# Optimization experiments

Measured on AMD Instinct MI355X. Metric: run time of the kernel, lower is better.

The kernel has to match this reference:

```python
import jax, jax.numpy as jnp
import numpy as np

B, N, F_IN, C_OUT = 128, 512, 2, 64
C_IN = F_IN + C_OUT           # 66, concat(input, state) feature dim
MLP_IN = (2 * 3 + 1) * C_IN   # order=2, support_len=3 -> 462


def _gcn(x, supports, W, b):
    """Diffusion conv: x [B,N,F]; for each support a, 2 diffusion orders."""
    outs = [x]
    for a in supports:
        x1 = jnp.einsum('bnf,nm->bmf', x, a)
        x2 = jnp.einsum('bnf,nm->bmf', x1, a)
        outs += [x1, x2]
    h = jnp.concatenate(outs, axis=2)  # [B, N, 7*F]
    return h @ W + b                   # Linear (dropout is eval-mode identity)


def setup_inputs() -> dict:
    key = jax.random.key(0)
    ks = jax.random.split(key, 12)
    return {
        'input': jax.random.normal(ks[0], (B, N, F_IN), dtype=jnp.float32),
        'state': jax.random.normal(ks[1], (B, N, C_OUT), dtype=jnp.float32),
        'A0':    jax.random.uniform(ks[2], (N, N), dtype=jnp.float32),
        'A1':    jax.random.uniform(ks[3], (N, N), dtype=jnp.float32),
        'nv1_1': jax.random.normal(ks[4], (N, 10), dtype=jnp.float32),
        'nv2_1': jax.random.normal(ks[5], (10, N), dtype=jnp.float32),
        'W1':    jax.random.normal(ks[6], (MLP_IN, 2 * C_OUT), dtype=jnp.float32) * 0.02,
        'b1':    jnp.zeros((2 * C_OUT,), dtype=jnp.float32),
        'nv1_2': jax.random.normal(ks[7], (N, 10), dtype=jnp.float32),
        'nv2_2': jax.random.normal(ks[8], (10, N), dtype=jnp.float32),
        'W2':    jax.random.normal(ks[9], (MLP_IN, C_OUT), dtype=jnp.float32) * 0.02,
        'b2':    jnp.zeros((C_OUT,), dtype=jnp.float32),
    }


def reference(input, state, A0, A1, nv1_1, nv2_1, W1, b1, nv1_2, nv2_2, W2, b2):
    c_out = state.shape[-1]
    # gcn_1: adaptive adjacency + diffusion conv, then sigmoid gating split into r,u
    adp1 = jax.nn.softmax(jax.nn.relu(nv1_1 @ nv2_1), axis=1)
    x = jnp.concatenate([input, state], axis=2)
    value = jax.nn.sigmoid(_gcn(x, [A0, A1, adp1], W1, b1))
    r, u = value[..., :c_out], value[..., c_out:]
    # gcn_2: candidate state
    adp2 = jax.nn.softmax(jax.nn.relu(nv1_2 @ nv2_2), axis=1)
    x2 = jnp.concatenate([input, r * state], axis=2)
    c = jnp.tanh(_gcn(x2, [A0, A1, adp2], W2, b2))
    return u * state + (1.0 - u) * c
```

## Files before the change

kernel.cpp:

```cpp
#include <hip/hip_runtime.h>
#include <math.h>

#define NN 512
#define BB 128
#define CIN 66
#define QQ (BB*CIN)
#define AN ((size_t)NN*NN)
#define HB 480
#define KTOT 480

typedef unsigned short ushort_t;
typedef __attribute__((ext_vector_type(8))) short short8;
typedef __attribute__((ext_vector_type(8))) unsigned short us8;
typedef __attribute__((ext_vector_type(4))) float f32x4;
typedef __attribute__((ext_vector_type(4))) unsigned short us4;

__device__ __forceinline__ size_t pidx(int b, int frow, int n) {
    return ((size_t)(b * 30 + (frow >> 4)) << 13) + ((size_t)(n >> 3) << 7)
         + ((frow & 15) << 3) + (n & 7);
}

__device__ __forceinline__ ushort_t f2bf(float f) {
    unsigned u = __float_as_uint(f);
    u += 0x7FFF + ((u >> 16) & 1);
    return (ushort_t)(u >> 16);
}
__device__ __forceinline__ float bf2f(ushort_t h) {
    return __uint_as_float(((unsigned)h) << 16);
}
__device__ __forceinline__ void split_bf(float f, ushort_t& hi, ushort_t& lo) {
    hi = f2bf(f);
    lo = f2bf(f - bf2f(hi));
}
__device__ __forceinline__ void gload_lds16(const void* g, void* l) {
    __builtin_amdgcn_global_load_lds(
        (const __attribute__((address_space(1))) unsigned*)g,
        (__attribute__((address_space(3))) unsigned*)l, 16, 0, 0);
}

__global__ __launch_bounds__(512) void adp_kernel(const float* __restrict__ nv1,
                                                  const float* __restrict__ nv2,
                                                  float* __restrict__ adp) {
    int n = blockIdx.x;
    int m = threadIdx.x;
    float z = 0.f;
#pragma unroll
    for (int k = 0; k < 10; k++) z = fmaf(nv1[n * 10 + k], nv2[k * NN + m], z);
    z = fmaxf(z, 0.f);

    __shared__ float sred[8];
    int wid  = threadIdx.x >> 6;
    int lane = threadIdx.x & 63;

    float v = z;
#pragma unroll
    for (int off = 32; off; off >>= 1) v = fmaxf(v, __shfl_down(v, off, 64));
    if (lane == 0) sred[wid] = v;
    __syncthreads();
    float zmax = sred[0];
#pragma unroll
    for (int i = 1; i < 8; i++) zmax = fmaxf(zmax, sred[i]);

    float e = __expf(z - zmax);
    __syncthreads();
    v = e;
#pragma unroll
    for (int off = 32; off; off >>= 1) v += __shfl_down(v, off, 64);
    if (lane == 0) sred[wid] = v;
    __syncthreads();
    float tot = 0.f;
#pragma unroll
    for (int i = 0; i < 8; i++) tot += sred[i];

    adp[n * NN + m] = e / tot;
}

__global__ __launch_bounds__(256) void asplit_kernel(const float* __restrict__ A0,
                                                     const float* __restrict__ A1,
                                                     const float* __restrict__ P1,
                                                     const float* __restrict__ P2,
                                                     ushort_t* __restrict__ Ahi,
                                                     ushort_t* __restrict__ Alo) {
    __shared__ float t[32][33];
    int s = blockIdx.z;
    const float* src = (s == 0) ? A0 : (s == 1) ? A1 : (s == 2) ? P1 : P2;
    int m0 = blockIdx.x * 32, k0 = blockIdx.y * 32;
    int tx = threadIdx.x & 31, ty = threadIdx.x >> 5;
#pragma unroll
    for (int r = 0; r < 32; r += 8)
        t[ty + r][tx] = src[(size_t)(k0 + ty + r) * NN + m0 + tx];
    __syncthreads();
#pragma unroll
    for (int r = 0; r < 32; r += 8) {
        int m = m0 + ty + r, k = k0 + tx;
        float v = t[tx][ty + r];
        ushort_t h, l; split_bf(v, h, l);
        int mt = m >> 4, l15 = m & 15;
        int kt = k >> 5, quad = (k >> 3) & 3, j = k & 7;
        size_t o = ((((size_t)s * 16 + kt) * 32 + mt) * 64 + quad * 16 + l15) * 8 + j;
        Ahi[o] = h; Alo[o] = l;
    }
}

template <int COUT>
__global__ __launch_bounds__(256) void wtprep_kernel(const float* __restrict__ W,
                                                     ushort_t* __restrict__ Wth,
                                                     ushort_t* __restrict__ Wtl) {
    int j = blockIdx.x;
    for (int k = threadIdx.x; k < KTOT; k += 256) {
        float v = (k < 462) ? W[(size_t)k * COUT + j] : 0.f;
        ushort_t h, l; split_bf(v, h, l);
        Wth[(size_t)j * KTOT + k] = h;
        Wtl[(size_t)j * KTOT + k] = l;
    }
}

__global__ __launch_bounds__(256) void buildx_kernel(const float* __restrict__ inp,
                                                     const float* __restrict__ st,
                                                     ushort_t* __restrict__ Xh,
                                                     ushort_t* __restrict__ Xl) {
    int gid = blockIdx.x * 256 + threadIdx.x;
    int ch  = gid & 63;
    int c   = (gid >> 6) % CIN;
    int b   = gid / (64 * CIN);
    int n0  = ch * 8;
    us8 h8, l8;
#pragma unroll
    for (int r = 0; r < 8; r++) {
        int n = n0 + r;
        float v = (c < 2) ? inp[((size_t)b * NN + n) * 2 + c]
                          : st[((size_t)b * NN + n) * 64 + (c - 2)];
        ushort_t h, l; split_bf(v, h, l);
        h8[r] = h; l8[r] = l;
    }
    size_t o = pidx(b, c, n0);
    *(us8*)&Xh[o] = h8;
    *(us8*)&Xl[o] = l8;
}

template <int HOP>
__global__ __launch_bounds__(256) void diff_mfma(const ushort_t* __restrict__ Aph,
                                                 const ushort_t* __restrict__ Apl,
                                                 ushort_t* Xh, ushort_t* Xl, int s2) {
    const int tid  = threadIdx.x;
    const int lane = tid & 63, w = tid >> 6;
    const int quad = lane >> 4, l15 = lane & 15;
    const int q0 = blockIdx.x * 128, m0 = blockIdx.y * 128;
    const int sz = blockIdx.z;
    const int sup = (sz < 2) ? sz : s2;
    const int roff_in = (HOP == 1) ? 0 : 66 + 132 * sz;
    const int wm = w & 1, wq = w >> 1;

    const ushort_t* xph[4];
    const ushort_t* xpl[4];
#pragma unroll
    for (int qt = 0; qt < 4; qt++) {
        int q = q0 + wq * 64 + qt * 16 + l15;
        int b = q / 66, c = q - 66 * b;
        int frow = roff_in + c;
        size_t off = ((size_t)(b * 30 + (frow >> 4)) << 13) + ((frow & 15) << 3)
                   + (size_t)quad * 128;
        xph[qt] = Xh + off;
        xpl[qt] = Xl + off;
    }
    const size_t abase = (size_t)sup * 262144;
    const int mtg0 = (m0 >> 4) + wm * 4;

    f32x4 acc[4][4] = {};
    short8 ahA[4], alA[4], xhA[4], xlA[4];
    short8 ahB[4], alB[4], xhB[4], xlB[4];

#define DLOAD(kt, ah, al, xh, xl)                                                  \
    {                                                                              \
        _Pragma("unroll")                                                          \
        for (int t = 0; t < 4; t++) {                                              \
            size_t fo = abase + ((size_t)(kt) * 32 + mtg0 + t) * 512 + lane * 8;   \
            ah[t] = *(const short8*)&Aph[fo];                                      \
            al[t] = *(const short8*)&Apl[fo];                                      \
            xh[t] = *(const short8*)&xph[t][(kt) * 512];                           \
            xl[t] = *(const short8*)&xpl[t][(kt) * 512];                           \
        }                                                                          \
    }
#define DMFMA(ah, al, xh, xl)                                                                      \
    {                                                                                              \
        _Pragma("unroll")                                                                          \
        for (int mt = 0; mt < 4; mt++) {                                                           \
            _Pragma("unroll")                                                                      \
            for (int qt = 0; qt < 4; qt++) {                                                       \
                acc[mt][qt] = __builtin_amdgcn_mfma_f32_16x16x32_bf16(ah[mt], xh[qt], acc[mt][qt], 0, 0, 0); \
                acc[mt][qt] = __builtin_amdgcn_mfma_f32_16x16x32_bf16(ah[mt], xl[qt], acc[mt][qt], 0, 0, 0); \
                acc[mt][qt] = __builtin_amdgcn_mfma_f32_16x16x32_bf16(al[mt], xh[qt], acc[mt][qt], 0, 0, 0); \
                acc[mt][qt] = __builtin_amdgcn_mfma_f32_16x16x32_bf16(al[mt], xl[qt], acc[mt][qt], 0, 0, 0); \
            }                                                                                      \
        }                                                                                          \
    }

    DLOAD(0, ahA, alA, xhA, xlA);
    for (int kt = 0; kt < 16; kt += 2) {
        DLOAD(kt + 1, ahB, alB, xhB, xlB);
        DMFMA(ahA, alA, xhA, xlA);
        if (kt + 2 < 16) DLOAD(kt + 2, ahA, alA, xhA, xlA);
        DMFMA(ahB, alB, xhB, xlB);
    }
#undef DLOAD
#undef DMFMA

    const int rowo = (HOP == 1) ? 66 + 132 * sz : 132 + 132 * sz;
#pragma unroll
    for (int qt = 0; qt < 4; qt++) {
        int q = q0 + wq * 64 + qt * 16 + l15;
        int b = q / 66, c = q - 66 * b;
        int frow = rowo + c;
#pragma unroll
        for (int mt = 0; mt < 4; mt++) {
            int n = m0 + wm * 64 + mt * 16 + quad * 4;
            us4 h4, l4;
#pragma unroll
            for (int r = 0; r < 4; r++) {
                ushort_t h, l; split_bf(acc[mt][qt][r], h, l);
                h4[r] = h; l4[r] = l;
            }
            size_t o = pidx(b, frow, n);
            *(us4*)&Xh[o] = h4;
            *(us4*)&Xl[o] = l4;
        }
    }
}

template <int COUT, int LAYER, int BM>
__global__ __launch_bounds__(256) void proj_mfma(const ushort_t* XhC, const ushort_t* XlC,
                                                 const ushort_t* __restrict__ Wth,
                                                 const ushort_t* __restrict__ Wtl,
                                                 const float* __restrict__ bias,
                                                 const float* __restrict__ state,
                                                 float* U,
                                                 ushort_t* Xhw, ushort_t* Xlw,
                                                 float* __restrict__ out) {
    __shared__ ushort_t sAh[BM * 32];
    __shared__ ushort_t sAl[BM * 32];
    __shared__ ushort_t sBh[COUT * 32];
    __shared__ ushort_t sBl[COUT * 32];
    constexpr int PB = COUT / 64;
    const int tid  = threadIdx.x;
    const int lane = tid & 63, w = tid >> 6;
    const int quad = lane >> 4, l15 = lane & 15;
    const int b = blockIdx.y, n0 = blockIdx.x * BM;
    const int wn = (COUT == 128) ? (w & 1) : w;
    const int wj = (COUT == 128) ? (w >> 1) : 0;
    const int kp = tid & 15, n8 = tid >> 4;

    size_t boff[PB]; int lB[PB];
#pragma unroll
    for (int p = 0; p < PB; p++) {
        int cid = p * 256 + tid;
        lB[p]   = cid * 8;
        boff[p] = (size_t)(cid >> 2) * KTOT + (cid & 3) * 8;
    }

    f32x4 acc[4][4] = {};

    for (int k0 = 0; k0 < KTOT; k0 += 32) {
        __syncthreads();
#pragma unroll
        for (int pass = 0; pass < BM / 128; pass++) {
            int np0 = (n8 + pass * 16) * 8;
            int kk  = k0 + 2 * kp;
            size_t o = pidx(b, kk, n0 + np0);
            us8 h0 = *(const us8*)&XhC[o];
            us8 h1 = *(const us8*)&XhC[o + 8];
            us8 l0 = *(const us8*)&XlC[o];
            us8 l1 = *(const us8*)&XlC[o + 8];
            int g = kp >> 2, ko = (2 * kp) & 7;
#pragma unroll
            for (int j2 = 0; j2 < 8; j2++) {
                int n   = np0 + j2;
                int idx = n * 32 + ((g ^ ((n >> 1) & 3)) << 3) + ko;
                *(unsigned*)&sAh[idx] = (unsigned)h0[j2] | ((unsigned)h1[j2] << 16);
                *(unsigned*)&sAl[idx] = (unsigned)l0[j2] | ((unsigned)l1[j2] << 16);
            }
        }
#pragma unroll
        for (int p = 0; p < PB; p++) {
            gload_lds16(Wth + boff[p] + k0, sBh + lB[p]);
            gload_lds16(Wtl + boff[p] + k0, sBl + lB[p]);
        }
        __syncthreads();
        short8 ah[4], al[4], bh[4], bl[4];
#pragma unroll
        for (int t = 0; t < 4; t++) {
            int an  = wn * 64 + t * 16 + l15;
            int ago = (quad ^ ((an >> 1) & 3)) << 3;
            ah[t] = *(const short8*)&sAh[an * 32 + ago];
            al[t] = *(const short8*)&sAl[an * 32 + ago];
            int brow = wj * 64 + t * 16 + l15;
            bh[t] = *(const short8*)&sBh[brow * 32 + quad * 8];
            bl[t] = *(const short8*)&sBl[brow * 32 + quad * 8];
        }
#pragma unroll
        for (int nt = 0; nt < 4; nt++)
#pragma unroll
            for (int jt = 0; jt < 4; jt++) {
                acc[nt][jt] = __builtin_amdgcn_mfma_f32_16x16x32_bf16(ah[nt], bh[jt], acc[nt][jt], 0, 0, 0);
                acc[nt][jt] = __builtin_amdgcn_mfma_f32_16x16x32_bf16(ah[nt], bl[jt], acc[nt][jt], 0, 0, 0);
                acc[nt][jt] = __builtin_amdgcn_mfma_f32_16x16x32_bf16(al[nt], bh[jt], acc[nt][jt], 0, 0, 0);
                acc[nt][jt] = __builtin_amdgcn_mfma_f32_16x16x32_bf16(al[nt], bl[jt], acc[nt][jt], 0, 0, 0);
            }
    }

#pragma unroll
    for (int jt = 0; jt < 4; jt++) {
        int j = wj * 64 + jt * 16 + l15;
        float bj = bias[j];
#pragma unroll
        for (int nt = 0; nt < 4; nt++) {
            int nb = n0 + wn * 64 + nt * 16 + quad * 4;
            f32x4 z = acc[nt][jt];
#pragma unroll
            for (int r = 0; r < 4; r++) z[r] += bj;
            if (LAYER == 1) {
#pragma unroll
                for (int r = 0; r < 4; r++) z[r] = 1.f / (1.f + __expf(-z[r]));
                if (j < 64) {
                    us4 h4, l4;
#pragma unroll
                    for (int r = 0; r < 4; r++) {
                        float x2 = z[r] * state[((size_t)b * NN + nb + r) * 64 + j];
                        ushort_t h, l; split_bf(x2, h, l);
                        h4[r] = h; l4[r] = l;
                    }
                    size_t o = pidx(b, 2 + j, nb);
                    *(us4*)&Xhw[o] = h4;
                    *(us4*)&Xlw[o] = l4;
                } else {
                    *(f32x4*)&U[((size_t)b * 64 + j - 64) * NN + nb] = z;
                }
            } else {
                f32x4 u4 = *(const f32x4*)&U[((size_t)b * 64 + j) * NN + nb];
#pragma unroll
                for (int r = 0; r < 4; r++) {
                    float c = tanhf(z[r]);
                    float s = state[((size_t)b * NN + nb + r) * 64 + j];
                    out[((size_t)b * NN + nb + r) * 64 + j] = u4[r] * s + (1.f - u4[r]) * c;
                }
            }
        }
    }
}

extern "C" void kernel_launch(void* const* d_in, const int* in_sizes, int n_in,
                              void* d_out, int out_size, void* d_ws, size_t ws_size,
                              hipStream_t stream) {
    const float* input = (const float*)d_in[0];
    const float* state = (const float*)d_in[1];
    const float* A0    = (const float*)d_in[2];
    const float* A1    = (const float*)d_in[3];
    const float* nv1_1 = (const float*)d_in[4];
    const float* nv2_1 = (const float*)d_in[5];
    const float* W1    = (const float*)d_in[6];
    const float* b1    = (const float*)d_in[7];
    const float* nv1_2 = (const float*)d_in[8];
    const float* nv2_2 = (const float*)d_in[9];
    const float* W2    = (const float*)d_in[10];
    const float* b2    = (const float*)d_in[11];
    float* out = (float*)d_out;

    char* p = (char*)d_ws;
    auto alloc = [&](size_t bytes) { void* r = (void*)p; p += (bytes + 255) & ~(size_t)255; return r; };
    float*    ADP1 = (float*)alloc(AN * 4);
    float*    ADP2 = (float*)alloc(AN * 4);
    ushort_t* Ahi  = (ushort_t*)alloc(4 * AN * 2);
    ushort_t* Alo  = (ushort_t*)alloc(4 * AN * 2);
    ushort_t* Xh   = (ushort_t*)alloc((size_t)BB * HB * NN * 2);
    ushort_t* Xl   = (ushort_t*)alloc((size_t)BB * HB * NN * 2);
    ushort_t* Wt1h = (ushort_t*)alloc((size_t)128 * KTOT * 2);
    ushort_t* Wt1l = (ushort_t*)alloc((size_t)128 * KTOT * 2);
    ushort_t* Wt2h = (ushort_t*)alloc((size_t)64 * KTOT * 2);
    ushort_t* Wt2l = (ushort_t*)alloc((size_t)64 * KTOT * 2);
    float*    U    = (float*)alloc((size_t)BB * 64 * NN * 4);

    adp_kernel<<<NN, NN, 0, stream>>>(nv1_1, nv2_1, ADP1);
    adp_kernel<<<NN, NN, 0, stream>>>(nv1_2, nv2_2, ADP2);
    asplit_kernel<<<dim3(16, 16, 4), 256, 0, stream>>>(A0, A1, ADP1, ADP2, Ahi, Alo);
    wtprep_kernel<128><<<128, 256, 0, stream>>>(W1, Wt1h, Wt1l);
    wtprep_kernel<64><<<64, 256, 0, stream>>>(W2, Wt2h, Wt2l);
    buildx_kernel<<<BB * CIN * 64 / 256, 256, 0, stream>>>(input, state, Xh, Xl);

    dim3 gd(QQ / 128, NN / 128, 3);
    diff_mfma<1><<<gd, 256, 0, stream>>>(Ahi, Alo, Xh, Xl, 2);
    diff_mfma<2><<<gd, 256, 0, stream>>>(Ahi, Alo, Xh, Xl, 2);
    proj_mfma<128, 1, 128><<<dim3(NN / 128, BB), 256, 0, stream>>>(Xh, Xl, Wt1h, Wt1l, b1, state,
                                                                   U, Xh, Xl, nullptr);
    diff_mfma<1><<<gd, 256, 0, stream>>>(Ahi, Alo, Xh, Xl, 3);
    diff_mfma<2><<<gd, 256, 0, stream>>>(Ahi, Alo, Xh, Xl, 3);
    proj_mfma<64, 2, 256><<<dim3(NN / 256, BB), 256, 0, stream>>>(Xh, Xl, Wt2h, Wt2l, b2, state,
                                                                  U, nullptr, nullptr, out);
}
```

Before: 469.9 us.

## Fuse both diffusion hops into one kernel keeping hop-1 result in LDS

Replaces the two per-hop diffusion kernels with one fused kernel in which each block covers 32 (batch,channel) columns across all 512 nodes. The hop-1 result is kept in shared memory and fed straight into hop 2, which saves a launch and a global reread of X1. In exchange the block tile is narrower, so each loaded A fragment is reused across fewer columns and A traffic rises. The software double-buffered prefetch is also dropped, and the large LDS footprint may limit occupancy.

```diff
diff --git a/kernel.cpp b/kernel.cpp
--- a/kernel.cpp
+++ b/kernel.cpp
@@ -138,93 +138,127 @@
     *(us8*)&Xl[o] = l8;
 }
 
-template <int HOP>
-__global__ __launch_bounds__(256) void diff_mfma(const ushort_t* __restrict__ Aph,
-                                                 const ushort_t* __restrict__ Apl,
-                                                 ushort_t* Xh, ushort_t* Xl, int s2) {
+__global__ __launch_bounds__(512, 4) void diff_fused(const ushort_t* __restrict__ Aph,
+                                                     const ushort_t* __restrict__ Apl,
+                                                     ushort_t* Xh, ushort_t* Xl, int s2) {
+    __shared__ ushort_t sX1h[32 * 520];
+    __shared__ ushort_t sX1l[32 * 520];
     const int tid  = threadIdx.x;
     const int lane = tid & 63, w = tid >> 6;
     const int quad = lane >> 4, l15 = lane & 15;
-    const int q0 = blockIdx.x * 128, m0 = blockIdx.y * 128;
+    const int q0 = blockIdx.x * 32;
     const int sz = blockIdx.z;
     const int sup = (sz < 2) ? sz : s2;
-    const int roff_in = (HOP == 1) ? 0 : 66 + 132 * sz;
-    const int wm = w & 1, wq = w >> 1;
-
-    const ushort_t* xph[4];
-    const ushort_t* xpl[4];
-#pragma unroll
-    for (int qt = 0; qt < 4; qt++) {
-        int q = q0 + wq * 64 + qt * 16 + l15;
+    const size_t abase = (size_t)sup * 262144;
+    const int mtg0 = w * 4;
+
+    const ushort_t* xph[2];
+    const ushort_t* xpl[2];
+    int bq[2], cq[2];
+#pragma unroll
+    for (int qt = 0; qt < 2; qt++) {
+        int q = q0 + qt * 16 + l15;
         int b = q / 66, c = q - 66 * b;
-        int frow = roff_in + c;
-        size_t off = ((size_t)(b * 30 + (frow >> 4)) << 13) + ((frow & 15) << 3)
+        bq[qt] = b; cq[qt] = c;
+        size_t off = ((size_t)(b * 30 + (c >> 4)) << 13) + ((c & 15) << 3)
                    + (size_t)quad * 128;
         xph[qt] = Xh + off;
         xpl[qt] = Xl + off;
     }
-    const size_t abase = (size_t)sup * 262144;
-    const int mtg0 = (m0 >> 4) + wm * 4;
-
-    f32x4 acc[4][4] = {};
-    short8 ahA[4], alA[4], xhA[4], xlA[4];
-    short8 ahB[4], alB[4], xhB[4], xlB[4];
-
-#define DLOAD(kt, ah, al, xh, xl)                                                  \
-    {                                                                              \
-        _Pragma("unroll")                                                          \
-        for (int t = 0; t < 4; t++) {                                              \
-            size_t fo = abase + ((size_t)(kt) * 32 + mtg0 + t) * 512 + lane * 8;   \
-            ah[t] = *(const short8*)&Aph[fo];                                      \
-            al[t] = *(const short8*)&Apl[fo];                                      \
-            xh[t] = *(const short8*)&xph[t][(kt) * 512];                           \
-            xl[t] = *(const short8*)&xpl[t][(kt) * 512];                           \
-        }                                                                          \
-    }
-#define DMFMA(ah, al, xh, xl)                                                                      \
+
+#define DMFMA2(ACC, AH, AL, XH, XL)                                                                \
     {                                                                                              \
         _Pragma("unroll")                                                                          \
         for (int mt = 0; mt < 4; mt++) {                                                           \
             _Pragma("unroll")                                                                      \
-            for (int qt = 0; qt < 4; qt++) {                                                       \
-                acc[mt][qt] = __builtin_amdgcn_mfma_f32_16x16x32_bf16(ah[mt], xh[qt], acc[mt][qt], 0, 0, 0); \
-                acc[mt][qt] = __builtin_amdgcn_mfma_f32_16x16x32_bf16(ah[mt], xl[qt], acc[mt][qt], 0, 0, 0); \
-                acc[mt][qt] = __builtin_amdgcn_mfma_f32_16x16x32_bf16(al[mt], xh[qt], acc[mt][qt], 0, 0, 0); \
-                acc[mt][qt] = __builtin_amdgcn_mfma_f32_16x16x32_bf16(al[mt], xl[qt], acc[mt][qt], 0, 0, 0); \
+            for (int qt = 0; qt < 2; qt++) {                                                       \
+                ACC[mt][qt] = __builtin_amdgcn_mfma_f32_16x16x32_bf16(AH[mt], XH[qt], ACC[mt][qt], 0, 0, 0); \
+                ACC[mt][qt] = __builtin_amdgcn_mfma_f32_16x16x32_bf16(AH[mt], XL[qt], ACC[mt][qt], 0, 0, 0); \
+                ACC[mt][qt] = __builtin_amdgcn_mfma_f32_16x16x32_bf16(AL[mt], XH[qt], ACC[mt][qt], 0, 0, 0); \
+                ACC[mt][qt] = __builtin_amdgcn_mfma_f32_16x16x32_bf16(AL[mt], XL[qt], ACC[mt][qt], 0, 0, 0); \
             }                                                                                      \
         }                                                                                          \
     }
 
-    DLOAD(0, ahA, alA, xhA, xlA);
-    for (int kt = 0; kt < 16; kt += 2) {
-        DLOAD(kt + 1, ahB, alB, xhB, xlB);
-        DMFMA(ahA, alA, xhA, xlA);
-        if (kt + 2 < 16) DLOAD(kt + 2, ahA, alA, xhA, xlA);
-        DMFMA(ahB, alB, xhB, xlB);
-    }
-#undef DLOAD
-#undef DMFMA
-
-    const int rowo = (HOP == 1) ? 66 + 132 * sz : 132 + 132 * sz;
-#pragma unroll
-    for (int qt = 0; qt < 4; qt++) {
-        int q = q0 + wq * 64 + qt * 16 + l15;
-        int b = q / 66, c = q - 66 * b;
-        int frow = rowo + c;
-#pragma unroll
-        for (int mt = 0; mt < 4; mt++) {
-            int n = m0 + wm * 64 + mt * 16 + quad * 4;
-            us4 h4, l4;
-#pragma unroll
-            for (int r = 0; r < 4; r++) {
-                ushort_t h, l; split_bf(acc[mt][qt][r], h, l);
-                h4[r] = h; l4[r] = l;
-            }
-            size_t o = pidx(b, frow, n);
-            *(us4*)&Xh[o] = h4;
-            *(us4*)&Xl[o] = l4;
-        }
-    }
+    {
+        f32x4 acc[4][2] = {};
+        for (int kt = 0; kt < 16; kt++) {
+            short8 ah[4], al[4], xh2[2], xl2[2];
+#pragma unroll
+            for (int t = 0; t < 4; t++) {
+                size_t fo = abase + ((size_t)kt * 32 + mtg0 + t) * 512 + lane * 8;
+                ah[t] = *(const short8*)&Aph[fo];
+                al[t] = *(const short8*)&Apl[fo];
+            }
+#pragma unroll
+            for (int qt = 0; qt < 2; qt++) {
+                xh2[qt] = *(const short8*)&xph[qt][(size_t)kt * 512];
+                xl2[qt] = *(const short8*)&xpl[qt][(size_t)kt * 512];
+            }
+            DMFMA2(acc, ah, al, xh2, xl2);
+        }
+        const int rowo = 66 + 132 * sz;
+#pragma unroll
+        for (int qt = 0; qt < 2; qt++) {
+            int qloc = qt * 16 + l15;
+            int frow = rowo + cq[qt];
+#pragma unroll
+            for (int mt = 0; mt < 4; mt++) {
+                int n = w * 64 + mt * 16 + quad * 4;
+                us4 h4, l4;
+#pragma unroll
+                for (int r = 0; r < 4; r++) {
+                    ushort_t h, l; split_bf(acc[mt][qt][r], h, l);
+                    h4[r] = h; l4[r] = l;
+                }
+                *(us4*)&sX1h[qloc * 520 + n] = h4;
+                *(us4*)&sX1l[qloc * 520 + n] = l4;
+                size_t o = pidx(bq[qt], frow, n);
+                *(us4*)&Xh[o] = h4;
+                *(us4*)&Xl[o] = l4;
+            }
+        }
+    }
+    __syncthreads();
+
+    {
+        f32x4 acc[4][2] = {};
+        for (int kt = 0; kt < 16; kt++) {
+            short8 ah[4], al[4], bh2[2], bl2[2];
+#pragma unroll
+            for (int t = 0; t < 4; t++) {
+                size_t fo = abase + ((size_t)kt * 32 + mtg0 + t) * 512 + lane * 8;
+                ah[t] = *(const short8*)&Aph[fo];
+                al[t] = *(const short8*)&Apl[fo];
+            }
+#pragma unroll
+            for (int qt = 0; qt < 2; qt++) {
+                int idx = (qt * 16 + l15) * 520 + kt * 32 + quad * 8;
+                bh2[qt] = *(const short8*)&sX1h[idx];
+                bl2[qt] = *(const short8*)&sX1l[idx];
+            }
+            DMFMA2(acc, ah, al, bh2, bl2);
+        }
+        const int rowo = 132 + 132 * sz;
+#pragma unroll
+        for (int qt = 0; qt < 2; qt++) {
+            int frow = rowo + cq[qt];
+#pragma unroll
+            for (int mt = 0; mt < 4; mt++) {
+                int n = w * 64 + mt * 16 + quad * 4;
+                us4 h4, l4;
+#pragma unroll
+                for (int r = 0; r < 4; r++) {
+                    ushort_t h, l; split_bf(acc[mt][qt][r], h, l);
+                    h4[r] = h; l4[r] = l;
+                }
+                size_t o = pidx(bq[qt], frow, n);
+                *(us4*)&Xh[o] = h4;
+                *(us4*)&Xl[o] = l4;
+            }
+        }
+    }
+#undef DMFMA2
 }
 
 template <int COUT, int LAYER, int BM>
@@ -385,13 +419,11 @@
     wtprep_kernel<64><<<64, 256, 0, stream>>>(W2, Wt2h, Wt2l);
     buildx_kernel<<<BB * CIN * 64 / 256, 256, 0, stream>>>(input, state, Xh, Xl);
 
-    dim3 gd(QQ / 128, NN / 128, 3);
-    diff_mfma<1><<<gd, 256, 0, stream>>>(Ahi, Alo, Xh, Xl, 2);
-    diff_mfma<2><<<gd, 256, 0, stream>>>(Ahi, Alo, Xh, Xl, 2);
+    dim3 gf(QQ / 32, 1, 3);
+    diff_fused<<<gf, 512, 0, stream>>>(Ahi, Alo, Xh, Xl, 2);
     proj_mfma<128, 1, 128><<<dim3(NN / 128, BB), 256, 0, stream>>>(Xh, Xl, Wt1h, Wt1l, b1, state,
                                                                    U, Xh, Xl, nullptr);
-    diff_mfma<1><<<gd, 256, 0, stream>>>(Ahi, Alo, Xh, Xl, 3);
-    diff_mfma<2><<<gd, 256, 0, stream>>>(Ahi, Alo, Xh, Xl, 3);
+    diff_fused<<<gf, 512, 0, stream>>>(Ahi, Alo, Xh, Xl, 3);
     proj_mfma<64, 2, 256><<<dim3(NN / 256, BB), 256, 0, stream>>>(Xh, Xl, Wt2h, Wt2l, b2, state,
                                                                   U, nullptr, nullptr, out);
 }
```

Result: faster. 417.7 us (-11.1%).
